# Optimization experiments

Measured on AMD Instinct MI355X. Metric: run time of the kernel, lower is better.

The kernel has to match this reference:

```python
import jax, jax.numpy as jnp
import numpy as np

B, LQ, C = 2, 21760, 256
NH, NL, NP = 8, 4, 4
HD = C // NH  # 32
SPATIAL = np.array([[128, 128], [64, 64], [32, 32], [16, 16]], dtype=np.int64)
START = np.array([0, 16384, 20480, 21504], dtype=np.int64)


def setup_inputs() -> dict:
    key = jax.random.key(0)
    ks = jax.random.split(key, 12)
    inp = {
        "query": jax.random.normal(ks[0], (B, LQ, C), jnp.float32),
        "reference_points": jax.random.uniform(ks[1], (B, LQ, NL, 2), jnp.float32),
        "input_flatten": jax.random.normal(ks[2], (B, LQ, C), jnp.float32),
        "input_spatial_shapes": jnp.asarray(SPATIAL),
        "input_level_start_index": jnp.asarray(START),
        # learned params (random small init so offsets stay reasonable)
        "W_off": jax.random.normal(ks[3], (C, NH * NL * NP * 2), jnp.float32) * 0.01,
        "b_off": jax.random.normal(ks[4], (NH * NL * NP * 2,), jnp.float32) * 0.5,
        "W_attn": jax.random.normal(ks[5], (C, NH * NL * NP), jnp.float32) * 0.02,
        "b_attn": jnp.zeros((NH * NL * NP,), jnp.float32),
        "W_val": jax.random.normal(ks[6], (C, C), jnp.float32) * (1.0 / np.sqrt(C)),
        "b_val": jnp.zeros((C,), jnp.float32),
        "W_out": jax.random.normal(ks[7], (C, C), jnp.float32) * (1.0 / np.sqrt(C)),
        "b_out": jnp.zeros((C,), jnp.float32),
    }
    return inp


def _bilinear_sample(v, loc, H, W):
    """v: (BH, H*W, D); loc: (BH, Q, P, 2) in [0,1] (x, y).
    F.grid_sample bilinear, padding_mode='zeros', align_corners=False.
    Returns (BH, Q, P, D)."""
    BH, Q, P, _ = loc.shape
    x = loc[..., 0] * W - 0.5
    y = loc[..., 1] * H - 0.5
    x0 = jnp.floor(x)
    y0 = jnp.floor(y)
    wx1 = x - x0
    wy1 = y - y0

    def corner(xi, yi, w):
        valid = (xi >= 0) & (xi < W) & (yi >= 0) & (yi < H)
        xi_c = jnp.clip(xi, 0, W - 1).astype(jnp.int32)
        yi_c = jnp.clip(yi, 0, H - 1).astype(jnp.int32)
        idx = (yi_c * W + xi_c).reshape(BH, Q * P)
        g = jnp.take_along_axis(v, idx[..., None], axis=1).reshape(BH, Q, P, -1)
        return g * (w * valid)[..., None]

    out = corner(x0, y0, (1.0 - wx1) * (1.0 - wy1))
    out = out + corner(x0 + 1.0, y0, wx1 * (1.0 - wy1))
    out = out + corner(x0, y0 + 1.0, (1.0 - wx1) * wy1)
    out = out + corner(x0 + 1.0, y0 + 1.0, wx1 * wy1)
    return out


def ms_deform_attn(query, reference_points, input_flatten, shapes_np,
                   W_off, b_off, W_attn, b_attn, W_val, b_val, W_out, b_out):
    Bq, Lq, _ = query.shape
    Len_in = input_flatten.shape[1]
    # value projection -> (B*NH, Len_in, HD)
    value = input_flatten @ W_val + b_val
    value = value.reshape(Bq, Len_in, NH, HD).transpose(0, 2, 1, 3).reshape(Bq * NH, Len_in, HD)
    # sampling offsets / attention weights
    offsets = (query @ W_off + b_off).reshape(Bq, Lq, NH, NL, NP, 2)
    attn = jax.nn.softmax((query @ W_attn + b_attn).reshape(Bq, Lq, NH, NL * NP), axis=-1)
    attn = attn.reshape(Bq, Lq, NH, NL, NP)
    # normalizer is (W_l, H_l) per level, matching (x, y) coordinate order
    normalizer = jnp.stack([jnp.asarray(shapes_np[:, 1], jnp.float32),
                            jnp.asarray(shapes_np[:, 0], jnp.float32)], axis=-1)  # (NL, 2)
    loc = reference_points[:, :, None, :, None, :] + offsets / normalizer[None, None, None, :, None, :]
    # (B, Lq, NH, NL, NP, 2) -> (B, NH, Lq, NL, NP, 2) -> (B*NH, Lq, NL, NP, 2)
    loc = loc.transpose(0, 2, 1, 3, 4, 5).reshape(Bq * NH, Lq, NL, NP, 2)
    attn_bh = attn.transpose(0, 2, 1, 3, 4).reshape(Bq * NH, Lq, NL, NP)

    out = jnp.zeros((Bq * NH, Lq, HD), value.dtype)
    start = 0
    for lvl in range(NL):
        Hc, Wc = int(shapes_np[lvl, 0]), int(shapes_np[lvl, 1])
        v_l = value[:, start:start + Hc * Wc]            # (BH, H*W, D)
        samp = _bilinear_sample(v_l, loc[:, :, lvl], Hc, Wc)  # (BH, Lq, P, D)
        out = out + jnp.einsum('bqpd,bqp->bqd', samp, attn_bh[:, :, lvl])
        start += Hc * Wc
    out = out.reshape(Bq, NH, Lq, HD).transpose(0, 2, 1, 3).reshape(Bq, Lq, C)
    return out @ W_out + b_out


def reference(query, reference_points, input_flatten, input_spatial_shapes,
              input_level_start_index, W_off, b_off, W_attn, b_attn,
              W_val, b_val, W_out, b_out):
    shapes_np = np.asarray(input_spatial_shapes)  # static level shapes
    return ms_deform_attn(query, reference_points, input_flatten, shapes_np,
                          W_off, b_off, W_attn, b_attn, W_val, b_val, W_out, b_out)
```

## Files before the change

### kernel.cpp

```cpp
#include <hip/hip_runtime.h>
#include <hip/hip_fp16.h>
#include <type_traits>

#define LQ 21760
#define MROWS 43520
#define LEN 21760

typedef __attribute__((ext_vector_type(8))) _Float16 half8;
typedef __attribute__((ext_vector_type(4))) float f32x4;

__device__ __forceinline__ uint pkh(float a, float b) {
  auto v = __builtin_amdgcn_cvt_pkrtz(a, b);
  return __builtin_bit_cast(uint, v);
}
__device__ __forceinline__ ushort h16(float x) {
  return __half_as_ushort(__float2half(x));
}
__device__ __forceinline__ float hlo(uint u) {
  return __half2float(__ushort_as_half((ushort)(u & 0xffffu)));
}
__device__ __forceinline__ float hhi(uint u) {
  return __half2float(__ushort_as_half((ushort)(u >> 16)));
}

__device__ __forceinline__ int swz8(int row, int k8) {
  return row * 32 + ((k8 ^ (row & 3) ^ ((row >> 2) & 3)) << 3);
}

template <int BN, bool SPLIT, typename AT, typename OT>
__device__ __forceinline__ void gemm_body(
    const AT* __restrict__ A, int lda, const ushort* __restrict__ WT,
    const float* __restrict__ bias, const float* __restrict__ bias2,
    OT* __restrict__ Cout, int ldc, ushort* __restrict__ C2, int mblk,
    ushort* Asb, ushort* Bsb) {
  constexpr int WN = BN / 4;
  constexpr int NI = WN / 16;
  constexpr int BSTEP = (BN * 4) / 512;
  const int tid = threadIdx.x;
  const int m0 = mblk * 128;
  const int w = tid >> 6, wm = w >> 2, wn = w & 3;
  const int l = tid & 63, lr = l & 15, lk = l >> 4;
  const int arow = tid >> 2, ak8 = tid & 3;

  f32x4 acc[4][NI];
#pragma unroll
  for (int mi = 0; mi < 4; ++mi)
#pragma unroll
    for (int ni = 0; ni < NI; ++ni) acc[mi][ni] = {0.f, 0.f, 0.f, 0.f};

  float4 aF0, aF1;
  uint4 aR;
  uint4 bR[BSTEP];

  auto loadA = [&](int k0) {
    const AT* src = A + (size_t)(m0 + arow) * lda + k0 + ak8 * 8;
    if constexpr (std::is_same_v<AT, float>) {
      aF0 = *(const float4*)src;
      aF1 = *(const float4*)(src + 4);
    } else {
      aR = *(const uint4*)src;
    }
  };
  auto loadB = [&](int k0) {
#pragma unroll
    for (int i = 0; i < BSTEP; ++i) {
      int s = tid + i * 512;
      bR[i] = *(const uint4*)(WT + (size_t)(s >> 2) * 256 + k0 + (s & 3) * 8);
    }
  };
  auto writeLDS = [&](int cur) {
    ushort* Ab = Asb + cur * (128 * 32);
    ushort* Bb = Bsb + cur * (BN * 32);
    uint4 pk;
    if constexpr (std::is_same_v<AT, float>)
      pk = make_uint4(pkh(aF0.x, aF0.y), pkh(aF0.z, aF0.w),
                      pkh(aF1.x, aF1.y), pkh(aF1.z, aF1.w));
    else
      pk = aR;
    *(uint4*)&Ab[swz8(arow, ak8)] = pk;
#pragma unroll
    for (int i = 0; i < BSTEP; ++i) {
      int s = tid + i * 512;
      *(uint4*)&Bb[swz8(s >> 2, s & 3)] = bR[i];
    }
  };

  loadA(0);
  loadB(0);
#pragma unroll
  for (int ks = 0; ks < 8; ++ks) {
    const int cur = ks & 1;
    writeLDS(cur);
    __syncthreads();
    if (ks < 7) {
      loadA((ks + 1) * 32);
      loadB((ks + 1) * 32);
    }
    const ushort* Ab = Asb + cur * (128 * 32);
    const ushort* Bb = Bsb + cur * (BN * 32);
    half8 af[4], bfr[NI];
#pragma unroll
    for (int mi = 0; mi < 4; ++mi)
      af[mi] = *(const half8*)&Ab[swz8(wm * 64 + mi * 16 + lr, lk)];
#pragma unroll
    for (int ni = 0; ni < NI; ++ni)
      bfr[ni] = *(const half8*)&Bb[swz8(wn * WN + ni * 16 + lr, lk)];
#pragma unroll
    for (int mi = 0; mi < 4; ++mi)
#pragma unroll
      for (int ni = 0; ni < NI; ++ni)
        acc[mi][ni] = __builtin_amdgcn_mfma_f32_16x16x32_f16(
            af[mi], bfr[ni], acc[mi][ni], 0, 0, 0);
  }
#pragma unroll
  for (int mi = 0; mi < 4; ++mi) {
#pragma unroll
    for (int ni = 0; ni < NI; ++ni) {
      int col = wn * WN + ni * 16 + lr;
      float bs;
      if constexpr (SPLIT)
        bs = (col < 256) ? bias[col] : bias2[col - 256];
      else
        bs = bias[col];
      int row = m0 + wm * 64 + mi * 16 + lk * 4;
#pragma unroll
      for (int r = 0; r < 4; ++r) {
        float v = acc[mi][ni][r] + bs;
        if constexpr (SPLIT) {
          if (col < 256)
            ((ushort*)Cout)[(size_t)(row + r) * 256 + col] = h16(v);
          else
            C2[(size_t)(row + r) * 128 + col - 256] = h16(v);
        } else if constexpr (std::is_same_v<OT, ushort>) {
          Cout[(size_t)(row + r) * ldc + col] = h16(v);
        } else {
          Cout[(size_t)(row + r) * ldc + col] = v;
        }
      }
    }
  }
}

__global__ __launch_bounds__(512) void gemm_front(
    const float* __restrict__ inpf, const ushort* __restrict__ WTv,
    const float* __restrict__ bval, ushort* __restrict__ value16,
    const float* __restrict__ query, const ushort* __restrict__ WTol,
    const float* __restrict__ boff, const float* __restrict__ battn,
    ushort* __restrict__ off16, ushort* __restrict__ logit16) {
  __shared__ ushort Asb[2 * 128 * 32];
  __shared__ ushort Bsb[2 * 384 * 32];
  int bid = blockIdx.x;
  if (bid < 340) {
    gemm_body<256, false, float, ushort>(inpf, 256, WTv, bval, nullptr,
                                         value16, 256, nullptr, bid, Asb, Bsb);
  } else {
    gemm_body<384, true, float, ushort>(query, 256, WTol, boff, battn, off16,
                                        256, logit16, bid - 340, Asb, Bsb);
  }
}

__global__ __launch_bounds__(512) void gemm_out(
    const ushort* __restrict__ midb, const ushort* __restrict__ WTu,
    const float* __restrict__ bout, float* __restrict__ outp) {
  __shared__ ushort Asb[2 * 128 * 32];
  __shared__ ushort Bsb[2 * 256 * 32];
  gemm_body<256, false, ushort, float>(midb, 512, WTu, bout, nullptr, outp,
                                       256, nullptr, blockIdx.x, Asb, Bsb);
}

__global__ __launch_bounds__(256) void wt_cvt_all(
    const float* __restrict__ Wval, const float* __restrict__ Woff,
    const float* __restrict__ Wattn, const float* __restrict__ Wout,
    ushort* __restrict__ WTv, ushort* __restrict__ WTol,
    ushort* __restrict__ WTu) {
  int i = blockIdx.x * 256 + threadIdx.x;
  if (i < 65536) {
    int n = i >> 8, k = i & 255;
    WTv[i] = h16(Wval[(size_t)k * 256 + n]);
  } else if (i < 163840) {
    int j = i - 65536;
    int n = j >> 8, k = j & 255;
    float s = (n < 256) ? Woff[(size_t)k * 256 + n] : Wattn[(size_t)k * 128 + n - 256];
    WTol[j] = h16(s);
  } else {
    int j = i - 163840;
    int n = j >> 8, k = j & 255;
    WTu[j] = h16(Wout[(size_t)k * 256 + n]);
  }
}

__global__ __launch_bounds__(256) void msda_sample(
    const ushort* __restrict__ off16,
    const ushort* __restrict__ logit16,
    const float* __restrict__ refpts,
    const ushort* __restrict__ value,
    ushort* __restrict__ midb) {
  __shared__ float prs[64][16];
  __shared__ float refs[32][4][2];
  __shared__ int tix[1024][4];
  __shared__ uint twp[1024][2];

  const int bid = blockIdx.x;
  const int grp = bid & 7;
  const int sub = bid >> 3;
  const int b = grp >> 2;
  const int hp = grp & 3;
  const int q0 = sub * 32;
  const int tid = threadIdx.x;
  const size_t fqB = (size_t)b * LQ + q0;

  {
    int q = tid >> 3, r = tid & 7;
    refs[q][r >> 1][r & 1] = refpts[(fqB + q) * 8 + r];
  }
  if (tid < 64) {
    int q = tid >> 1, hh = tid & 1;
    int h = hp * 2 + hh;
    const uint4* lp = (const uint4*)(logit16 + (fqB + q) * 128 + h * 16);
    uint4 p0 = lp[0], p1 = lp[1];
    float v[16] = {hlo(p0.x), hhi(p0.x), hlo(p0.y), hhi(p0.y),
                   hlo(p0.z), hhi(p0.z), hlo(p0.w), hhi(p0.w),
                   hlo(p1.x), hhi(p1.x), hlo(p1.y), hhi(p1.y),
                   hlo(p1.z), hhi(p1.z), hlo(p1.w), hhi(p1.w)};
    float m = v[0];
#pragma unroll
    for (int i = 1; i < 16; ++i) m = fmaxf(m, v[i]);
    float s = 0.f;
#pragma unroll
    for (int i = 0; i < 16; ++i) { v[i] = __expf(v[i] - m); s += v[i]; }
    float inv = 1.0f / s;
#pragma unroll
    for (int i = 0; i < 16; ++i) prs[tid][i] = v[i] * inv;
  }
  __syncthreads();

#pragma unroll
  for (int i = 0; i < 4; ++i) {
    int t = tid + i * 256;
    int q = t >> 5;
    int hh = (t >> 4) & 1;
    int lp_ = t & 15;
    int lvl = lp_ >> 2;
    int h = hp * 2 + hh;
    uint op = ((const uint*)off16)[(fqB + q) * 128 + h * 16 + lp_];
    float ox = hlo(op), oy = hhi(op);
    float aw = prs[q * 2 + hh][lp_];
    float rx = refs[q][lvl][0], ry = refs[q][lvl][1];
    int Wl = 128 >> lvl;
    int st = (lvl == 0) ? 0 : ((lvl == 1) ? 16384 : ((lvl == 2) ? 20480 : 21504));
    float fW = (float)Wl;
    float invW = 1.0f / fW;
    float x = (rx + ox * invW) * fW - 0.5f;
    float y = (ry + oy * invW) * fW - 0.5f;
    float x0f = floorf(x), y0f = floorf(y);
    float wx1 = x - x0f, wy1 = y - y0f;
    float wx0 = 1.f - wx1, wy0 = 1.f - wy1;
    int x0 = (int)x0f, y0 = (int)y0f;
    int x1 = x0 + 1, y1 = y0 + 1;
    bool vx0 = (x0 >= 0) & (x0 < Wl), vx1 = (x1 >= 0) & (x1 < Wl);
    bool vy0 = (y0 >= 0) & (y0 < Wl), vy1 = (y1 >= 0) & (y1 < Wl);
    int xc0 = min(max(x0, 0), Wl - 1), xc1 = min(max(x1, 0), Wl - 1);
    int yc0 = min(max(y0, 0), Wl - 1), yc1 = min(max(y1, 0), Wl - 1);
    int base = st * 256 + h * 32;
    int g16 = t >> 4;
    int slot = (t & ~15) | ((t + g16) & 15);
    float w00 = (vx0 && vy0) ? wx0 * wy0 * aw : 0.f;
    float w10 = (vx1 && vy0) ? wx1 * wy0 * aw : 0.f;
    float w01 = (vx0 && vy1) ? wx0 * wy1 * aw : 0.f;
    float w11 = (vx1 && vy1) ? wx1 * wy1 * aw : 0.f;
    tix[slot][0] = base + (yc0 * Wl + xc0) * 256;
    tix[slot][1] = base + (yc0 * Wl + xc1) * 256;
    tix[slot][2] = base + (yc1 * Wl + xc0) * 256;
    tix[slot][3] = base + (yc1 * Wl + xc1) * 256;
    twp[slot][0] = pkh(w00, w10);
    twp[slot][1] = pkh(w01, w11);
  }
  __syncthreads();

  const int g = tid >> 2;
  const int dl = tid & 3;
  const ushort* vb = value + (size_t)b * LEN * 256 + dl * 8;
  float a0 = 0.f, a1 = 0.f, a2 = 0.f, a3 = 0.f;
  float a4 = 0.f, a5 = 0.f, a6 = 0.f, a7 = 0.f;
  const int tb = g * 16;

#define FMAMIX(ACC, WP, U, OPSEL) \
  asm("v_fma_mix_f32 %0, %1, %2, %0 " OPSEL : "+v"(ACC) : "v"(WP), "v"(U))
#define CORNER(U, WPW, WS)                                              \
  FMAMIX(a0, WPW, (U).x, "op_sel:[" WS ",0,0] op_sel_hi:[1,1,0]");      \
  FMAMIX(a1, WPW, (U).x, "op_sel:[" WS ",1,0] op_sel_hi:[1,1,0]");      \
  FMAMIX(a2, WPW, (U).y, "op_sel:[" WS ",0,0] op_sel_hi:[1,1,0]");      \
  FMAMIX(a3, WPW, (U).y, "op_sel:[" WS ",1,0] op_sel_hi:[1,1,0]");      \
  FMAMIX(a4, WPW, (U).z, "op_sel:[" WS ",0,0] op_sel_hi:[1,1,0]");      \
  FMAMIX(a5, WPW, (U).z, "op_sel:[" WS ",1,0] op_sel_hi:[1,1,0]");      \
  FMAMIX(a6, WPW, (U).w, "op_sel:[" WS ",0,0] op_sel_hi:[1,1,0]");      \
  FMAMIX(a7, WPW, (U).w, "op_sel:[" WS ",1,0] op_sel_hi:[1,1,0]")

#pragma unroll 4
  for (int t = 0; t < 16; ++t) {
    int slot = tb + ((t + g) & 15);
    int4 ix = *(const int4*)&tix[slot][0];
    uint2 wp = *(const uint2*)&twp[slot][0];
    uint4 u0 = *(const uint4*)(vb + ix.x);
    uint4 u1 = *(const uint4*)(vb + ix.y);
    uint4 u2 = *(const uint4*)(vb + ix.z);
    uint4 u3 = *(const uint4*)(vb + ix.w);
    CORNER(u0, wp.x, "0");
    CORNER(u1, wp.x, "1");
    CORNER(u2, wp.y, "0");
    CORNER(u3, wp.y, "1");
  }
#undef CORNER
#undef FMAMIX

  const int q = g >> 1, h = hp * 2 + (g & 1);
  ushort* mp = midb + (fqB + q) * 512 + h * 32 + dl * 8;
  *(uint4*)mp = make_uint4(pkh(a0, a1), pkh(a2, a3), pkh(a4, a5), pkh(a6, a7));
}

extern "C" void kernel_launch(void* const* d_in, const int* in_sizes, int n_in,
                              void* d_out, int out_size, void* d_ws,
                              size_t ws_size, hipStream_t stream) {
  (void)in_sizes; (void)n_in; (void)out_size; (void)ws_size;
  const float* query = (const float*)d_in[0];
  const float* refp  = (const float*)d_in[1];
  const float* inpf  = (const float*)d_in[2];
  const float* Woff  = (const float*)d_in[5];
  const float* boff  = (const float*)d_in[6];
  const float* Wattn = (const float*)d_in[7];
  const float* battn = (const float*)d_in[8];
  const float* Wval  = (const float*)d_in[9];
  const float* bval  = (const float*)d_in[10];
  const float* Wout  = (const float*)d_in[11];
  const float* bout  = (const float*)d_in[12];

  ushort* value16 = (ushort*)d_ws;
  ushort* off16   = value16 + (size_t)MROWS * 256;
  ushort* logit16 = off16 + (size_t)MROWS * 256;
  ushort* WTv     = logit16 + (size_t)MROWS * 128;
  ushort* WTol    = WTv + 65536;
  ushort* WTu     = WTol + 98304;

  ushort* midb = (ushort*)d_out;

  wt_cvt_all<<<896, 256, 0, stream>>>(Wval, Woff, Wattn, Wout, WTv, WTol, WTu);

  gemm_front<<<680, 512, 0, stream>>>(inpf, WTv, bval, value16, query, WTol,
                                      boff, battn, off16, logit16);

  msda_sample<<<MROWS / 8, 256, 0, stream>>>(off16, logit16, refp, value16,
                                             midb);

  gemm_out<<<MROWS / 128, 512, 0, stream>>>(midb, WTu, bout, (float*)d_out);
}
```

Measured before the change: 131.7 us.

## Pack sample records into one uint4 and software-pipeline gathers in msda_sample

Replaces the separate index and weight shared arrays with a single 16-byte record per sample holding a byte base offset, packed x/y corner deltas and packed half weights. The gather loop is fully unrolled with explicit software pipelining: records are prefetched four ahead and corner loads are issued two ahead into a three-deep register ring. Launch bounds now request four blocks per SM. The goal is to hide gather latency and cut LDS traffic, at the cost of more registers per thread, which the occupancy hint may force into spills.

```diff
diff --git a/kernel.cpp b/kernel.cpp
--- a/kernel.cpp
+++ b/kernel.cpp
@@ -189,7 +189,7 @@
   }
 }
 
-__global__ __launch_bounds__(256) void msda_sample(
+__global__ __launch_bounds__(256, 4) void msda_sample(
     const ushort* __restrict__ off16,
     const ushort* __restrict__ logit16,
     const float* __restrict__ refpts,
@@ -197,8 +197,7 @@
     ushort* __restrict__ midb) {
   __shared__ float prs[64][16];
   __shared__ float refs[32][4][2];
-  __shared__ int tix[1024][4];
-  __shared__ uint twp[1024][2];
+  __shared__ uint4 trec[1024];
 
   const int bid = blockIdx.x;
   const int grp = bid & 7;
@@ -261,28 +260,25 @@
     bool vy0 = (y0 >= 0) & (y0 < Wl), vy1 = (y1 >= 0) & (y1 < Wl);
     int xc0 = min(max(x0, 0), Wl - 1), xc1 = min(max(x1, 0), Wl - 1);
     int yc0 = min(max(y0, 0), Wl - 1), yc1 = min(max(y1, 0), Wl - 1);
-    int base = st * 256 + h * 32;
     int g16 = t >> 4;
     int slot = (t & ~15) | ((t + g16) & 15);
     float w00 = (vx0 && vy0) ? wx0 * wy0 * aw : 0.f;
     float w10 = (vx1 && vy0) ? wx1 * wy0 * aw : 0.f;
     float w01 = (vx0 && vy1) ? wx0 * wy1 * aw : 0.f;
     float w11 = (vx1 && vy1) ? wx1 * wy1 * aw : 0.f;
-    tix[slot][0] = base + (yc0 * Wl + xc0) * 256;
-    tix[slot][1] = base + (yc0 * Wl + xc1) * 256;
-    tix[slot][2] = base + (yc1 * Wl + xc0) * 256;
-    tix[slot][3] = base + (yc1 * Wl + xc1) * 256;
-    twp[slot][0] = pkh(w00, w10);
-    twp[slot][1] = pkh(w01, w11);
+    uint ixB = (uint)((((st + yc0 * Wl + xc0) * 256) + h * 32) * 2);
+    uint dxy = (uint)((xc1 - xc0) * 512) | (uint)((yc1 - yc0) * Wl * 512);
+    trec[slot] = make_uint4(ixB, dxy, pkh(w00, w10), pkh(w01, w11));
   }
   __syncthreads();
 
   const int g = tid >> 2;
   const int dl = tid & 3;
-  const ushort* vb = value + (size_t)b * LEN * 256 + dl * 8;
+  const uint dlB = (uint)dl * 16u;
+  const char* vb0c = (const char*)(value + (size_t)b * (LEN * 256));
+  const int tb = g * 16;
   float a0 = 0.f, a1 = 0.f, a2 = 0.f, a3 = 0.f;
   float a4 = 0.f, a5 = 0.f, a6 = 0.f, a7 = 0.f;
-  const int tb = g * 16;
 
 #define FMAMIX(ACC, WP, U, OPSEL) \
   asm("v_fma_mix_f32 %0, %1, %2, %0 " OPSEL : "+v"(ACC) : "v"(WP), "v"(U))
@@ -296,20 +292,34 @@
   FMAMIX(a6, WPW, (U).w, "op_sel:[" WS ",0,0] op_sel_hi:[1,1,0]");      \
   FMAMIX(a7, WPW, (U).w, "op_sel:[" WS ",1,0] op_sel_hi:[1,1,0]")
 
-#pragma unroll 4
+#define LDREC(R, T) { (R) = trec[tb + (((T) + g) & 15)]; }
+#define ISSUE(R, S) {                                       \
+    uint dx_ = (R).y & 0x3ffu;                              \
+    uint dy_ = (R).y - dx_;                                 \
+    uint o0_ = (R).x + dlB;                                 \
+    uint o2_ = o0_ + dy_;                                   \
+    S[0] = *(const uint4*)(vb0c + o0_);                     \
+    S[1] = *(const uint4*)(vb0c + (o0_ + dx_));             \
+    S[2] = *(const uint4*)(vb0c + o2_);                     \
+    S[3] = *(const uint4*)(vb0c + (o2_ + dx_)); }
+#define ACCUM(R, S)                                         \
+  CORNER(S[0], (R).z, "0"); CORNER(S[1], (R).z, "1");       \
+  CORNER(S[2], (R).w, "0"); CORNER(S[3], (R).w, "1")
+
+  uint4 rec[5];
+  uint4 ld[3][4];
+  LDREC(rec[0], 0); LDREC(rec[1], 1); LDREC(rec[2], 2); LDREC(rec[3], 3);
+  ISSUE(rec[0], ld[0]);
+  ISSUE(rec[1], ld[1]);
+#pragma unroll
   for (int t = 0; t < 16; ++t) {
-    int slot = tb + ((t + g) & 15);
-    int4 ix = *(const int4*)&tix[slot][0];
-    uint2 wp = *(const uint2*)&twp[slot][0];
-    uint4 u0 = *(const uint4*)(vb + ix.x);
-    uint4 u1 = *(const uint4*)(vb + ix.y);
-    uint4 u2 = *(const uint4*)(vb + ix.z);
-    uint4 u3 = *(const uint4*)(vb + ix.w);
-    CORNER(u0, wp.x, "0");
-    CORNER(u1, wp.x, "1");
-    CORNER(u2, wp.y, "0");
-    CORNER(u3, wp.y, "1");
-  }
+    if (t < 14) { ISSUE(rec[(t + 2) % 5], ld[(t + 2) % 3]); }
+    if (t < 12) { LDREC(rec[(t + 4) % 5], t + 4); }
+    ACCUM(rec[t % 5], ld[t % 3]);
+  }
+#undef ACCUM
+#undef ISSUE
+#undef LDREC
 #undef CORNER
 #undef FMAMIX
 
```

After: 146.5 us. 1.11x slower.
